# Performance work log

Measured on AMD Instinct MI355X. Metric: run time of the kernel, lower is better.

## Reference

```python
import jax, jax.numpy as jnp
import numpy as np

T, B, D, H, MID, A = 512, 128, 256, 512, 512, 3


def setup_inputs() -> dict:
    key = jax.random.key(0)
    ks = jax.random.split(key, 16)
    kb = 1.0 / np.sqrt(H)

    def u(kk, shape):
        return jax.random.uniform(kk, shape, jnp.float32, -kb, kb)

    def lin(kk, fan_in, fan_out, std=0.05):
        k1, k2 = jax.random.split(kk)
        return (jax.random.normal(k1, (fan_out, fan_in), jnp.float32) * std,
                jnp.full((fan_out,), 1e-6, jnp.float32))

    aw0, ab0 = lin(ks[6], H + D, MID)
    aw1, ab1 = lin(ks[7], MID, MID)
    aw2, ab2 = lin(ks[8], MID, A, std=0.1 / np.sqrt(MID))
    cw0, cb0 = lin(ks[9], H + D, MID)
    cw1, cb1 = lin(ks[10], MID, MID)
    cw2, cb2 = lin(ks[11], MID, 1, std=0.5 / np.sqrt(MID))

    return {
        "state": jax.random.normal(ks[0], (T, B, D), jnp.float32),
        "hidden_state": jnp.zeros((B, H), jnp.float32),
        "cell_state": jnp.zeros((B, H), jnp.float32),
        "len_sequence": jax.random.randint(ks[1], (B,), 1, T + 1),
        "W_ih": u(ks[2], (4 * H, D)), "W_hh": u(ks[3], (4 * H, H)),
        "b_ih": u(ks[4], (4 * H,)), "b_hh": u(ks[5], (4 * H,)),
        "aw0": aw0, "ab0": ab0, "aw1": aw1, "ab1": ab1, "aw2": aw2, "ab2": ab2,
        "cw0": cw0, "cb0": cb0, "cw1": cw1, "cb1": cb1, "cw2": cw2, "cb2": cb2,
    }


def _pack_indices(len_sequence):
    # ragged packing: concat first len[b] timesteps of each batch row
    lens = np.asarray(len_sequence)
    return jnp.asarray(np.concatenate(
        [b * T + np.arange(l) for b, l in enumerate(lens)]))


def _mlp(x, w0, b0, w1, b1, w2, b2):
    h = jax.nn.relu(x @ w0.T + b0)
    h = jax.nn.relu(h @ w1.T + b1)
    return h @ w2.T + b2


def reference(state, hidden_state, cell_state, len_sequence,
              W_ih, W_hh, b_ih, b_hh,
              aw0, ab0, aw1, ab1, aw2, ab2,
              cw0, cb0, cw1, cb1, cw2, cb2):
    flat_idx = _pack_indices(len_sequence)

    def step(carry, x_t):
        h, c = carry
        gates = x_t @ W_ih.T + b_ih + h @ W_hh.T + b_hh
        i, f, g, o = jnp.split(gates, 4, axis=-1)
        c = jax.nn.sigmoid(f) * c + jax.nn.sigmoid(i) * jnp.tanh(g)
        h = jax.nn.sigmoid(o) * jnp.tanh(c)
        return (h, c), h

    _, hs = jax.lax.scan(step, (hidden_state, cell_state), state)  # [T,B,H]

    rnn_emb = hs.transpose(1, 0, 2).reshape(B * T, H)[flat_idx]      # [N,H]
    st = state.transpose(1, 0, 2).reshape(B * T, D)[flat_idx]        # [N,D]
    inp = jnp.concatenate([st, rnn_emb], axis=1)                     # [N,D+H]

    actor = jnp.tanh(_mlp(inp, aw0, ab0, aw1, ab1, aw2, ab2))
    critic = _mlp(inp, cw0, cb0, cw1, cb1, cw2, cb2)
    return actor, critic
```

## Files before the change

### kernel.cpp

```cpp
#include <hip/hip_runtime.h>
#include <stdint.h>


#define T_STEPS 512
#define BATCH   128
#define DDIM    256
#define HDIM    512

typedef __attribute__((ext_vector_type(8))) short bf16x8;
typedef __attribute__((ext_vector_type(4))) float f32x4;
typedef __attribute__((ext_vector_type(2))) unsigned long long u64x2;
typedef unsigned short u16;
typedef unsigned int   u32;
typedef unsigned long long u64;
typedef __attribute__((ext_vector_type(4))) u32 u32x4;

__device__ __forceinline__ u16 f2bf(float x){
  u32 u = __builtin_bit_cast(u32, x);
  u32 r = u + 0x7fffu + ((u >> 16) & 1u);
  return (u16)(r >> 16);
}
__device__ __forceinline__ float bf2f(u16 h){
  u32 u = ((u32)h) << 16;
  return __builtin_bit_cast(float, u);
}
__device__ __forceinline__ float sigm(float x){ return 1.f/(1.f + __expf(-x)); }
__device__ __forceinline__ float tanh_f(float x){ return 1.f - 2.f/(1.f + __expf(2.f*x)); }

__device__ __forceinline__ void async_ld16(const void* g, void* l){
  __builtin_amdgcn_global_load_lds(
      (const __attribute__((address_space(1))) u32*)g,
      (__attribute__((address_space(3))) u32*)l, 16, 0, 0);
}

__device__ __forceinline__ u32 ld_u32_sc0(const int* p){
  u32 v;
  asm volatile("global_load_dword %0, %1, off sc0\n\t"
               "s_waitcnt vmcnt(0)"
               : "=&v"(v) : "v"(p) : "memory");
  return v;
}
__device__ __forceinline__ void st_u32_sc0(int* p, u32 v){
  asm volatile("global_store_dword %0, %1, off sc0" :: "v"(p), "v"(v) : "memory");
}
__device__ __forceinline__ void ld2_b128_sc0_issue(const void* p0, const void* p1,
                                                   u32x4& A0, u32x4& A1){
  asm volatile("global_load_dwordx4 %0, %2, off sc0\n\t"
               "global_load_dwordx4 %1, %3, off sc0"
               : "=&v"(A0), "=&v"(A1) : "v"(p0), "v"(p1) : "memory");
}
__device__ __forceinline__ void ld2_b128_cc_issue(const void* p0, const void* p1,
                                                  u32x4& A0, u32x4& A1){
  asm volatile("global_load_dwordx4 %0, %2, off sc0 sc1\n\t"
               "global_load_dwordx4 %1, %3, off sc0 sc1"
               : "=&v"(A0), "=&v"(A1) : "v"(p0), "v"(p1) : "memory");
}

__global__ void sniff_kernel(const u16* __restrict__ b, int* __restrict__ mode){
  if (threadIdx.x == 0){
    int bad = 0;
    for (int i = 0; i < 64; i++){
      u16 x = b[2*i];
      int e = (x >> 7) & 0xFF;
      if (e < 0x60 || e > 0x85) bad++;
    }
    *mode = (bad > 16) ? 1 : 0;
  }
}

__global__ void cvt_kernel(const void* __restrict__ src, u16* __restrict__ dst,
                           int n, const int* __restrict__ mode){
  int i0 = (blockIdx.x*blockDim.x + threadIdx.x) * 8;
  if (i0 >= n) return;
  int m = *mode;
  if (m){
    const float* s = (const float*)src;
    if (i0 + 8 <= n){
      float4 a = *(const float4*)(s + i0);
      float4 b = *(const float4*)(s + i0 + 4);
      ushort4 oa, ob;
      oa.x=f2bf(a.x); oa.y=f2bf(a.y); oa.z=f2bf(a.z); oa.w=f2bf(a.w);
      ob.x=f2bf(b.x); ob.y=f2bf(b.y); ob.z=f2bf(b.z); ob.w=f2bf(b.w);
      *(ushort4*)(dst + i0) = oa;
      *(ushort4*)(dst + i0 + 4) = ob;
    } else {
      for (int i = i0; i < n; i++) dst[i] = f2bf(s[i]);
    }
  } else {
    const u16* s = (const u16*)src;
    if (i0 + 8 <= n){
      *(ushort4*)(dst + i0)     = *(const ushort4*)(s + i0);
      *(ushort4*)(dst + i0 + 4) = *(const ushort4*)(s + i0 + 4);
    } else {
      for (int i = i0; i < n; i++) dst[i] = s[i];
    }
  }
}

__global__ void scan_kernel(const int* __restrict__ lens, int* __restrict__ off){
  if (threadIdx.x == 0){
    int a = 0;
    for (int b = 0; b < BATCH; b++){ off[b] = a; a += lens[b]; }
    off[BATCH] = a;
  }
}

__global__ void pack_state_kernel(const u16* __restrict__ st_bf,
                                  const int* __restrict__ lens,
                                  const int* __restrict__ off,
                                  u16* __restrict__ inp){
  int r = blockIdx.x*4 + (threadIdx.x >> 6);
  int lane = threadIdx.x & 63;
  int b = r & (BATCH-1), t = r >> 7;
  if (t >= lens[b]) return;
  long row = (long)off[b] + t;
  ushort4 v = ((const ushort4*)(st_bf + (long)r*DDIM))[lane];
  ((ushort4*)(inp + row*768))[lane] = v;
}

__global__ void zero_out_kernel(void* __restrict__ out, int n,
                                const int* __restrict__ mode){
  int i = blockIdx.x*blockDim.x + threadIdx.x;
  if (i >= n) return;
  if (*mode) ((float*)out)[i] = 0.f; else ((u16*)out)[i] = 0;
}

__global__ __launch_bounds__(512, 1) void lstm_kernel(
    const u16* __restrict__ Whh, const u16* __restrict__ Wih,
    const u16* __restrict__ bih, const u16* __restrict__ bhh,
    const u16* __restrict__ cell0,
    const u16* __restrict__ state,
    u16* hbuf,
    u16* __restrict__ inp,
    const int* __restrict__ off, const int* __restrict__ lens,
    int* tags,
    int* probe)
{
  const int tid  = threadIdx.x;
  const int wave = tid >> 6;
  const int lane = tid & 63;
  const int g    = blockIdx.x & 7;
  const int s    = blockIdx.x >> 3;
  const int Sb   = s * 32;
  const int q    = lane >> 4;
  const int m16  = lane & 15;

  __shared__ u16  wlds[65536];
  __shared__ u16  hlds[8192];
  __shared__ float lds_acc[8][16][16];
  __shared__ float bias_l[128];
  __shared__ int   len_l[16];
  __shared__ int   off_l[16];
  __shared__ int   fast_l;

  if (wave == 0){
    if (lane == 0){
      st_u32_sc0(&probe[blockIdx.x], 0xC0FFEE00u | (u32)blockIdx.x);
      asm volatile("s_waitcnt vmcnt(0)" ::: "memory");
      st_u32_sc0(&probe[128 + blockIdx.x], 1u);
    }
    int seen = 1;
    if (lane < 16){
      int partner = 8*lane + g;
      seen = 0;
      for (int sp = 0; sp < (1 << 11); sp++){
        u32 tgv = ld_u32_sc0(&probe[128 + partner]);
        if (tgv == 1u){
          u32 v = ld_u32_sc0(&probe[partner]);
          if (v == (0xC0FFEE00u | (u32)partner)) seen = 1;
          break;
        }
      }
    }
    int okl = __all(seen != 0) ? 1 : 0;
    if (lane == 0){
      if (!okl)
        __hip_atomic_fetch_or(&probe[256], 1,
                              __ATOMIC_RELAXED, __HIP_MEMORY_SCOPE_AGENT);
      __hip_atomic_fetch_add(&probe[257], 1,
                             __ATOMIC_RELEASE, __HIP_MEMORY_SCOPE_AGENT);
      int sp2 = 0;
      while (__hip_atomic_load(&probe[257], __ATOMIC_ACQUIRE,
                               __HIP_MEMORY_SCOPE_AGENT) < 128){
        if (++sp2 >= (1 << 16)) break;
      }
      int bad = __hip_atomic_load(&probe[256], __ATOMIC_RELAXED,
                                  __HIP_MEMORY_SCOPE_AGENT);
      int cnt = __hip_atomic_load(&probe[257], __ATOMIC_RELAXED,
                                  __HIP_MEMORY_SCOPE_AGENT);
      fast_l = (!bad && cnt >= 128) ? 1 : 0;
    }
  }

  if (tid < 128){
    int gt = tid >> 5, jx = tid & 31;
    int cg = gt*HDIM + Sb + jx;
    bias_l[tid] = bf2f(bih[cg]) + bf2f(bhh[cg]);
  }
  if (tid < 16){ len_l[tid] = lens[g*16 + tid]; off_l[tid] = off[g*16 + tid]; }

  for (int i = 0; i < 16; i++){
    int ch = tid + 512*i;
    int w = ch >> 10;
    int rem = ch & 1023;
    int c = rem >> 6;
    int l = rem & 63;
    int col = (w >> 1)*HDIM + Sb + (w & 1)*16 + (l & 15);
    int k = c*32 + (l >> 4)*8;
    u64x2 v = *(const u64x2*)(Whh + (long)col*HDIM + k);
    *(u64x2*)(&wlds[(size_t)ch*8]) = v;
  }

  const int gate = wave >> 1;
  const int hf   = wave & 1;
  const int colg = gate*HDIM + Sb + hf*16 + m16;
  bf16x8 wih[8];
  {
    const u16* wb2 = Wih + (long)colg*DDIM + q*8;
    #pragma unroll
    for (int c = 0; c < 8; c++) wih[c] = *(const bf16x8*)(wb2 + c*32);
  }

  const int b_l = tid >> 5;
  const int j   = tid & 31;
  const int hx  = j >> 4;
  const int jj  = j & 15;
  float cval = bf2f(cell0[(g*16 + b_l)*HDIM + Sb + j]);

  const int m0 = tid, m1 = tid + 512;
  const int c0i = m0 >> 6, c1i = m1 >> 6;
  const int r0 = m0 & 15;
  const int k0 = c0i*32 + ((m0 & 63) >> 4)*8;
  const int k1 = c1i*32 + ((m1 & 63) >> 4)*8;

  int* tg = tags + g*16;

  __syncthreads();
  const int fast = fast_l;

  for (int t = 0; t < T_STEPS; t++){
    f32x4 acc  = {0.f, 0.f, 0.f, 0.f};
    f32x4 acc2 = {0.f, 0.f, 0.f, 0.f};
    bf16x8 xa[8];
    {
      const u16* xb = state + ((long)(t*BATCH + g*16 + m16))*DDIM + q*8;
      #pragma unroll
      for (int c = 0; c < 8; c++) xa[c] = *(const bf16x8*)(xb + c*32);
    }
    if (t > 0){
      int spins = 0;
      if (fast){
        for (;;){
          int tv = 0x7fffffff;
          if (lane < 16) tv = (int)ld_u32_sc0(&tg[lane]);
          if (__all(tv >= t)) break;
          if (++spins > (1 << 14)) break;
        }
      } else {
        for (;;){
          int tv = 0x7fffffff;
          if (lane < 16)
            tv = __hip_atomic_load(&tg[lane], __ATOMIC_RELAXED,
                                   __HIP_MEMORY_SCOPE_AGENT);
          if (__all(tv >= t)) break;
          if (++spins > (1 << 14)) break;
        }
      }
      asm volatile("" ::: "memory");
    }
    const u16* hp = hbuf + ((t & 1) ^ 1)*(BATCH*HDIM) + (size_t)g*16*HDIM;
    u32x4 A0, A1;
    if (fast) ld2_b128_sc0_issue(hp + r0*HDIM + k0, hp + r0*HDIM + k1, A0, A1);
    else      ld2_b128_cc_issue (hp + r0*HDIM + k0, hp + r0*HDIM + k1, A0, A1);
    #pragma unroll
    for (int c = 0; c < 8; c++)
      acc = __builtin_amdgcn_mfma_f32_16x16x32_bf16(xa[c], wih[c], acc, 0, 0, 0);
    asm volatile("s_waitcnt vmcnt(0)" ::: "memory");
    __builtin_amdgcn_sched_barrier(0);
    *(u32x4*)(&hlds[(size_t)m0*8]) = A0;
    *(u32x4*)(&hlds[(size_t)m1*8]) = A1;
    __syncthreads();
    #pragma unroll
    for (int cc = 0; cc < 8; cc++){
      bf16x8 a0 = *(const bf16x8*)(&hlds[(size_t)((2*cc    )*64 + lane)*8]);
      bf16x8 a1 = *(const bf16x8*)(&hlds[(size_t)((2*cc + 1)*64 + lane)*8]);
      bf16x8 w0 = *(const bf16x8*)(&wlds[(size_t)((wave*16 + 2*cc    )*64 + lane)*8]);
      bf16x8 w1 = *(const bf16x8*)(&wlds[(size_t)((wave*16 + 2*cc + 1)*64 + lane)*8]);
      acc  = __builtin_amdgcn_mfma_f32_16x16x32_bf16(a0, w0, acc,  0, 0, 0);
      acc2 = __builtin_amdgcn_mfma_f32_16x16x32_bf16(a1, w1, acc2, 0, 0, 0);
    }
    #pragma unroll
    for (int r = 0; r < 4; r++)
      lds_acc[wave][q*4 + r][m16] = acc[r] + acc2[r];
    __syncthreads();

    float iv = lds_acc[0 + hx][b_l][jj] + bias_l[ 0 + j];
    float fv = lds_acc[2 + hx][b_l][jj] + bias_l[32 + j];
    float gv = lds_acc[4 + hx][b_l][jj] + bias_l[64 + j];
    float ov = lds_acc[6 + hx][b_l][jj] + bias_l[96 + j];
    cval = sigm(fv)*cval + sigm(iv)*tanh_f(gv);
    float hv = sigm(ov)*tanh_f(cval);
    u16 hb16 = f2bf(hv);
    int nb = __shfl_down((int)hb16, 1);
    if ((j & 1) == 0){
      size_t hidx = (size_t)(t & 1)*(BATCH*HDIM) + (g*16 + b_l)*HDIM + Sb + j;
      u32 pair = (u32)hb16 | ((u32)(u16)nb << 16);
      if (fast) st_u32_sc0((int*)(hbuf + hidx), pair);
      else      __hip_atomic_store((u32*)(hbuf + hidx), pair,
                                   __ATOMIC_RELAXED, __HIP_MEMORY_SCOPE_AGENT);
    }
    __builtin_amdgcn_s_waitcnt(0);
    __syncthreads();
    if (tid == 0){
      if (fast) st_u32_sc0(&tg[s], (u32)(t + 1));
      else      __hip_atomic_store(&tg[s], t + 1,
                                   __ATOMIC_RELAXED, __HIP_MEMORY_SCOPE_AGENT);
    }
    if (t < len_l[b_l])
      inp[((long)(off_l[b_l] + t))*768 + DDIM + Sb + j] = hb16;
  }
}

__global__ __launch_bounds__(256) void gemm_kernel(
    const u16* __restrict__ A,
    const u16* __restrict__ W,
    const u16* __restrict__ bias,
    u16* __restrict__ C,
    int K)
{
  __shared__ u16 As[128*32];
  __shared__ u16 Bs[128*32];
  const int tid = threadIdx.x, wave = tid >> 6, lane = tid & 63;
  const int bm = blockIdx.x * 128;
  const int bn = blockIdx.y * 128;
  const int wr = (wave >> 1) * 64;
  const int wc = (wave & 1) * 64;
  const int q = lane >> 4, m16 = lane & 15;
  const int rsub = lane >> 2;
  const int ksub = (lane & 3) * 8;

  f32x4 acc[4][4] = {};

  for (int k0 = 0; k0 < K; k0 += 32){
    __syncthreads();
    #pragma unroll
    for (int i = 0; i < 2; i++){
      int rr = (i*4 + wave) * 16 + rsub;
      async_ld16(A + (long)(bm + rr)*K + k0 + ksub, As + (i*4 + wave)*512);
      async_ld16(W + (long)(bn + rr)*K + k0 + ksub, Bs + (i*4 + wave)*512);
    }
    __syncthreads();
    bf16x8 af[4], bfr[4];
    #pragma unroll
    for (int r = 0; r < 4; r++) af[r]  = *(const bf16x8*)(As + (wr + r*16 + m16)*32 + q*8);
    #pragma unroll
    for (int c = 0; c < 4; c++) bfr[c] = *(const bf16x8*)(Bs + (wc + c*16 + m16)*32 + q*8);
    #pragma unroll
    for (int r = 0; r < 4; r++)
      #pragma unroll
      for (int c = 0; c < 4; c++)
        acc[r][c] = __builtin_amdgcn_mfma_f32_16x16x32_bf16(af[r], bfr[c], acc[r][c], 0, 0, 0);
  }
  #pragma unroll
  for (int c = 0; c < 4; c++){
    int col = bn + wc + c*16 + m16;
    float bv = bf2f(bias[col]);
    #pragma unroll
    for (int r = 0; r < 4; r++){
      #pragma unroll
      for (int x = 0; x < 4; x++){
        int row = bm + wr + r*16 + q*4 + x;
        float v = acc[r][c][x] + bv;
        v = fmaxf(v, 0.f);
        C[(long)row*512 + col] = f2bf(v);
      }
    }
  }
}

__global__ void final_kernel(
    const u16* __restrict__ a2, const u16* __restrict__ c2,
    const u16* __restrict__ aw2, const u16* __restrict__ ab2,
    const u16* __restrict__ cw2, const u16* __restrict__ cb2,
    void* __restrict__ out, int base, int nvalid, int N,
    const int* __restrict__ mode)
{
  int lw = (blockIdx.x * blockDim.x + threadIdx.x) >> 6;
  int lane = threadIdx.x & 63;
  if (lw >= nvalid) return;
  int k = lane * 8;
  bf16x8 av = *(const bf16x8*)(a2 + (long)lw*512 + k);
  bf16x8 cv = *(const bf16x8*)(c2 + (long)lw*512 + k);
  bf16x8 w0 = *(const bf16x8*)(aw2 + k);
  bf16x8 w1 = *(const bf16x8*)(aw2 + 512 + k);
  bf16x8 w2 = *(const bf16x8*)(aw2 + 1024 + k);
  bf16x8 wc = *(const bf16x8*)(cw2 + k);
  float d0=0.f, d1=0.f, d2=0.f, dc=0.f;
  #pragma unroll
  for (int x = 0; x < 8; x++){
    float a  = bf2f((u16)av[x]);
    float cc = bf2f((u16)cv[x]);
    d0 += a  * bf2f((u16)w0[x]);
    d1 += a  * bf2f((u16)w1[x]);
    d2 += a  * bf2f((u16)w2[x]);
    dc += cc * bf2f((u16)wc[x]);
  }
  #pragma unroll
  for (int o = 32; o > 0; o >>= 1){
    d0 += __shfl_down(d0, o);
    d1 += __shfl_down(d1, o);
    d2 += __shfl_down(d2, o);
    dc += __shfl_down(dc, o);
  }
  if (lane == 0){
    int gr = base + lw;
    float r0 = tanh_f(d0 + bf2f(ab2[0]));
    float r1 = tanh_f(d1 + bf2f(ab2[1]));
    float r2 = tanh_f(d2 + bf2f(ab2[2]));
    float rc = dc + bf2f(cb2[0]);
    if (*mode){
      float* o = (float*)out;
      o[(long)gr*3 + 0] = r0; o[(long)gr*3 + 1] = r1; o[(long)gr*3 + 2] = r2;
      o[(long)3*N + gr] = rc;
    } else {
      u16* o = (u16*)out;
      o[(long)gr*3 + 0] = f2bf(r0); o[(long)gr*3 + 1] = f2bf(r1);
      o[(long)gr*3 + 2] = f2bf(r2);
      o[(long)3*N + gr] = f2bf(rc);
    }
  }
}

extern "C" void kernel_launch(void* const* d_in, const int* in_sizes, int n_in,
                              void* d_out, int out_size, void* d_ws, size_t ws_size,
                              hipStream_t stream)
{
  const void* state = d_in[0];
  const void* h0    = d_in[1];
  const void* c0    = d_in[2];
  const int*  lens  = (const int*)d_in[3];
  const void* Wih   = d_in[4];
  const void* Whh   = d_in[5];
  const void* bih   = d_in[6];
  const void* bhh   = d_in[7];
  const void* aw0   = d_in[8];
  const void* ab0   = d_in[9];
  const void* aw1   = d_in[10];
  const void* ab1   = d_in[11];
  const void* aw2   = d_in[12];
  const void* ab2   = d_in[13];
  const void* cw0   = d_in[14];
  const void* cb0   = d_in[15];
  const void* cw1   = d_in[16];
  const void* cb1   = d_in[17];
  const void* cw2   = d_in[18];
  const void* cb2   = d_in[19];
  (void)in_sizes; (void)n_in;

  const int N = out_size / 4;
  const int Np128 = (N + 127) & ~127;

  char* ws = (char*)d_ws;
  size_t cur = 0;
  auto alloc = [&](size_t bytes)->char*{
    char* p = ws + cur; cur += (bytes + 255) & ~(size_t)255; return p;
  };
  int* mode   = (int*)alloc(4);
  int* off    = (int*)alloc(129*4);
  int* tags   = (int*)alloc(128*4);
  int* probe  = (int*)alloc(512*4);
  u16* hbuf   = (u16*)alloc((size_t)2*BATCH*HDIM*2);
  u16* cbf    = (u16*)alloc((size_t)BATCH*HDIM*2);
  u16* wih_b  = (u16*)alloc((size_t)2048*256*2);
  u16* whh_b  = (u16*)alloc((size_t)2048*512*2);
  u16* bih_b  = (u16*)alloc(2048*2);
  u16* bhh_b  = (u16*)alloc(2048*2);
  u16* st_bf  = (u16*)alloc((size_t)T_STEPS*BATCH*DDIM*2);
  u16* wa0    = (u16*)alloc((size_t)512*768*2);
  u16* ba0    = (u16*)alloc(512*2);
  u16* wa1    = (u16*)alloc((size_t)512*512*2);
  u16* ba1    = (u16*)alloc(512*2);
  u16* wa2    = (u16*)alloc(1536*2);
  u16* ba2    = (u16*)alloc(256*2);
  u16* wc0    = (u16*)alloc((size_t)512*768*2);
  u16* bc0    = (u16*)alloc(512*2);
  u16* wc1    = (u16*)alloc((size_t)512*512*2);
  u16* bc1    = (u16*)alloc(512*2);
  u16* wc2    = (u16*)alloc(512*2);
  u16* bc2    = (u16*)alloc(256*2);
  u16* inp    = (u16*)alloc((size_t)Np128*768*2);

  sniff_kernel<<<1, 64, 0, stream>>>((const u16*)bih, mode);

  if (cur > ws_size){
    zero_out_kernel<<<(out_size + 255)/256, 256, 0, stream>>>(d_out, out_size, mode);
    return;
  }
  size_t rem = ws_size - cur;
  long CH_l = (long)((rem / 3) / (512*2)) & ~127L;
  int CH = (int)(CH_l > 8192 ? 8192 : CH_l);
  if (CH < 128){
    zero_out_kernel<<<(out_size + 255)/256, 256, 0, stream>>>(d_out, out_size, mode);
    return;
  }
  u16* bufA = (u16*)alloc((size_t)CH*512*2);
  u16* bufB = (u16*)alloc((size_t)CH*512*2);
  u16* bufC = (u16*)alloc((size_t)CH*512*2);

  auto cvt = [&](const void* src, u16* dst, int n){
    int thr = (n + 7) / 8;
    cvt_kernel<<<(thr + 255)/256, 256, 0, stream>>>(src, dst, n, mode);
  };
  cvt(Wih, wih_b, 2048*256);
  cvt(Whh, whh_b, 2048*512);
  cvt(bih, bih_b, 2048);
  cvt(bhh, bhh_b, 2048);
  cvt(h0,  hbuf + BATCH*HDIM, BATCH*HDIM);
  cvt(c0,  cbf, BATCH*HDIM);
  cvt(state, st_bf, T_STEPS*BATCH*DDIM);
  cvt(aw0, wa0, 512*768);  cvt(ab0, ba0, 512);
  cvt(aw1, wa1, 512*512);  cvt(ab1, ba1, 512);
  cvt(aw2, wa2, 1536);     cvt(ab2, ba2, 3);
  cvt(cw0, wc0, 512*768);  cvt(cb0, bc0, 512);
  cvt(cw1, wc1, 512*512);  cvt(cb1, bc1, 512);
  cvt(cw2, wc2, 512);      cvt(cb2, bc2, 1);

  hipMemsetAsync(tags, 0, 128*4, stream);
  hipMemsetAsync(probe, 0, 512*4, stream);
  scan_kernel<<<1, 64, 0, stream>>>(lens, off);
  pack_state_kernel<<<(T_STEPS*BATCH)/4, 256, 0, stream>>>(st_bf, lens, off, inp);

  lstm_kernel<<<128, 512, 0, stream>>>(whh_b, wih_b, bih_b, bhh_b, cbf, st_bf,
                                       hbuf, inp, off, lens, tags, probe);

  for (int cs = 0; cs < Np128; cs += CH){
    int rows = (Np128 - cs) < CH ? (Np128 - cs) : CH;
    int gm = rows / 128;
    dim3 gg(gm, 4);
    gemm_kernel<<<gg, 256, 0, stream>>>(inp + (long)cs*768, wa0, ba0, bufA, 768);
    gemm_kernel<<<gg, 256, 0, stream>>>(bufA,               wa1, ba1, bufB, 512);
    gemm_kernel<<<gg, 256, 0, stream>>>(inp + (long)cs*768, wc0, bc0, bufA, 768);
    gemm_kernel<<<gg, 256, 0, stream>>>(bufA,               wc1, bc1, bufC, 512);
    int nvalid = (N - cs) < rows ? (N - cs) : rows;
    if (nvalid > 0)
      final_kernel<<<(nvalid + 3)/4, 256, 0, stream>>>(bufB, bufC, wa2, ba2,
                                                       wc2, bc2, d_out, cs,
                                                       nvalid, N, mode);
  }
}
```

Baseline: 2.409 ms.

## Double-buffer GEMM LDS tiles and fuse actor/critic first-layer GEMMs

The GEMM kernel now double-buffers its LDS tiles, prefetching the next K-slice while MFMAs run on the current one. The actor and critic first-layer weights are stacked into one 1024-row matrix, so a single launch computes both hidden layers into a wider buffer. The second-layer GEMMs read their halves through a leading-dimension stride. This removes one launch per chunk and overlaps global loads with compute, at the cost of twice the LDS per block and a larger intermediate buffer, which shrinks the chunk size.

```diff
diff --git a/kernel.cpp b/kernel.cpp
--- a/kernel.cpp
+++ b/kernel.cpp
@@ -322,14 +322,14 @@
 }
 
 __global__ __launch_bounds__(256) void gemm_kernel(
-    const u16* __restrict__ A,
+    const u16* __restrict__ A, int lda,
     const u16* __restrict__ W,
     const u16* __restrict__ bias,
-    u16* __restrict__ C,
+    u16* __restrict__ C, int ldc,
     int K)
 {
-  __shared__ u16 As[128*32];
-  __shared__ u16 Bs[128*32];
+  __shared__ u16 As[2][128*32];
+  __shared__ u16 Bs[2][128*32];
   const int tid = threadIdx.x, wave = tid >> 6, lane = tid & 63;
   const int bm = blockIdx.x * 128;
   const int bn = blockIdx.y * 128;
@@ -340,26 +340,40 @@
   const int ksub = (lane & 3) * 8;
 
   f32x4 acc[4][4] = {};
-
-  for (int k0 = 0; k0 < K; k0 += 32){
-    __syncthreads();
-    #pragma unroll
-    for (int i = 0; i < 2; i++){
-      int rr = (i*4 + wave) * 16 + rsub;
-      async_ld16(A + (long)(bm + rr)*K + k0 + ksub, As + (i*4 + wave)*512);
-      async_ld16(W + (long)(bn + rr)*K + k0 + ksub, Bs + (i*4 + wave)*512);
-    }
-    __syncthreads();
+  const int nt = K >> 5;
+
+  #pragma unroll
+  for (int i = 0; i < 2; i++){
+    int rr = (i*4 + wave) * 16 + rsub;
+    async_ld16(A + (long)(bm + rr)*lda + ksub, As[0] + (i*4 + wave)*512);
+    async_ld16(W + (long)(bn + rr)*K   + ksub, Bs[0] + (i*4 + wave)*512);
+  }
+  asm volatile("s_waitcnt vmcnt(0)" ::: "memory");
+  __syncthreads();
+
+  for (int t = 0; t < nt; t++){
+    const int cur = t & 1;
+    if (t + 1 < nt){
+      int kk = (t + 1) << 5;
+      #pragma unroll
+      for (int i = 0; i < 2; i++){
+        int rr = (i*4 + wave) * 16 + rsub;
+        async_ld16(A + (long)(bm + rr)*lda + kk + ksub, As[cur ^ 1] + (i*4 + wave)*512);
+        async_ld16(W + (long)(bn + rr)*K   + kk + ksub, Bs[cur ^ 1] + (i*4 + wave)*512);
+      }
+    }
     bf16x8 af[4], bfr[4];
     #pragma unroll
-    for (int r = 0; r < 4; r++) af[r]  = *(const bf16x8*)(As + (wr + r*16 + m16)*32 + q*8);
-    #pragma unroll
-    for (int c = 0; c < 4; c++) bfr[c] = *(const bf16x8*)(Bs + (wc + c*16 + m16)*32 + q*8);
+    for (int r = 0; r < 4; r++) af[r]  = *(const bf16x8*)(As[cur] + (wr + r*16 + m16)*32 + q*8);
+    #pragma unroll
+    for (int c = 0; c < 4; c++) bfr[c] = *(const bf16x8*)(Bs[cur] + (wc + c*16 + m16)*32 + q*8);
     #pragma unroll
     for (int r = 0; r < 4; r++)
       #pragma unroll
       for (int c = 0; c < 4; c++)
         acc[r][c] = __builtin_amdgcn_mfma_f32_16x16x32_bf16(af[r], bfr[c], acc[r][c], 0, 0, 0);
+    asm volatile("s_waitcnt vmcnt(0)" ::: "memory");
+    __syncthreads();
   }
   #pragma unroll
   for (int c = 0; c < 4; c++){
@@ -372,7 +386,7 @@
         int row = bm + wr + r*16 + q*4 + x;
         float v = acc[r][c][x] + bv;
         v = fmaxf(v, 0.f);
-        C[(long)row*512 + col] = f2bf(v);
+        C[(long)row*ldc + col] = f2bf(v);
       }
     }
   }
@@ -476,14 +490,12 @@
   u16* bih_b  = (u16*)alloc(2048*2);
   u16* bhh_b  = (u16*)alloc(2048*2);
   u16* st_bf  = (u16*)alloc((size_t)T_STEPS*BATCH*DDIM*2);
-  u16* wa0    = (u16*)alloc((size_t)512*768*2);
-  u16* ba0    = (u16*)alloc(512*2);
+  u16* wst0   = (u16*)alloc((size_t)1024*768*2);
+  u16* bst0   = (u16*)alloc(1024*2);
   u16* wa1    = (u16*)alloc((size_t)512*512*2);
   u16* ba1    = (u16*)alloc(512*2);
   u16* wa2    = (u16*)alloc(1536*2);
   u16* ba2    = (u16*)alloc(256*2);
-  u16* wc0    = (u16*)alloc((size_t)512*768*2);
-  u16* bc0    = (u16*)alloc(512*2);
   u16* wc1    = (u16*)alloc((size_t)512*512*2);
   u16* bc1    = (u16*)alloc(512*2);
   u16* wc2    = (u16*)alloc(512*2);
@@ -497,13 +509,13 @@
     return;
   }
   size_t rem = ws_size - cur;
-  long CH_l = (long)((rem / 3) / (512*2)) & ~127L;
+  long CH_l = (long)(rem / (2048*2)) & ~127L;
   int CH = (int)(CH_l > 8192 ? 8192 : CH_l);
   if (CH < 128){
     zero_out_kernel<<<(out_size + 255)/256, 256, 0, stream>>>(d_out, out_size, mode);
     return;
   }
-  u16* bufA = (u16*)alloc((size_t)CH*512*2);
+  u16* bufA = (u16*)alloc((size_t)CH*1024*2);
   u16* bufB = (u16*)alloc((size_t)CH*512*2);
   u16* bufC = (u16*)alloc((size_t)CH*512*2);
 
@@ -518,10 +530,12 @@
   cvt(h0,  hbuf + BATCH*HDIM, BATCH*HDIM);
   cvt(c0,  cbf, BATCH*HDIM);
   cvt(state, st_bf, T_STEPS*BATCH*DDIM);
-  cvt(aw0, wa0, 512*768);  cvt(ab0, ba0, 512);
+  cvt(aw0, wst0, 512*768);
+  cvt(cw0, wst0 + (size_t)512*768, 512*768);
+  cvt(ab0, bst0, 512);
+  cvt(cb0, bst0 + 512, 512);
   cvt(aw1, wa1, 512*512);  cvt(ab1, ba1, 512);
   cvt(aw2, wa2, 1536);     cvt(ab2, ba2, 3);
-  cvt(cw0, wc0, 512*768);  cvt(cb0, bc0, 512);
   cvt(cw1, wc1, 512*512);  cvt(cb1, bc1, 512);
   cvt(cw2, wc2, 512);      cvt(cb2, bc2, 1);
 
@@ -536,11 +550,12 @@
   for (int cs = 0; cs < Np128; cs += CH){
     int rows = (Np128 - cs) < CH ? (Np128 - cs) : CH;
     int gm = rows / 128;
-    dim3 gg(gm, 4);
-    gemm_kernel<<<gg, 256, 0, stream>>>(inp + (long)cs*768, wa0, ba0, bufA, 768);
-    gemm_kernel<<<gg, 256, 0, stream>>>(bufA,               wa1, ba1, bufB, 512);
-    gemm_kernel<<<gg, 256, 0, stream>>>(inp + (long)cs*768, wc0, bc0, bufA, 768);
-    gemm_kernel<<<gg, 256, 0, stream>>>(bufA,               wc1, bc1, bufC, 512);
+    gemm_kernel<<<dim3(gm, 8), 256, 0, stream>>>(inp + (long)cs*768, 768,
+                                                 wst0, bst0, bufA, 1024, 768);
+    gemm_kernel<<<dim3(gm, 4), 256, 0, stream>>>(bufA, 1024,
+                                                 wa1, ba1, bufB, 512, 512);
+    gemm_kernel<<<dim3(gm, 4), 256, 0, stream>>>(bufA + 512, 1024,
+                                                 wc1, bc1, bufC, 512, 512);
     int nvalid = (N - cs) < rows ? (N - cs) : rows;
     if (nvalid > 0)
       final_kernel<<<(nvalid + 3)/4, 256, 0, stream>>>(bufB, bufC, wa2, ba2,
```

Result: faster. 2.323 ms (-3.6%).
